# Optimization experiments

Hardware: AMD Instinct MI355X
Metric: run time of the kernel (lower is better)

Reference implementation:

```python
import jax, jax.numpy as jnp
import numpy as np

B, N_IN, D_IN, N_OUT, D_OUT, ROUTINGS = 512, 1152, 8, 10, 16, 3


def squash(s, axis=-1):
    # scale = |s|^2 / (1 + |s|^2) / (|s| + 1e-8)
    norm = jnp.linalg.norm(s, axis=axis, keepdims=True)
    return (norm ** 2 / (1.0 + norm ** 2) / (norm + 1e-8)) * s


def setup_inputs() -> dict:
    key = jax.random.key(0)
    k1, k2 = jax.random.split(key)
    x = jax.random.normal(k1, (B, N_IN, D_IN), dtype=jnp.float32)
    weight = 0.01 * jax.random.normal(k2, (N_OUT, N_IN, D_OUT, D_IN), dtype=jnp.float32)
    return {"x": x, "weight": weight}


def reference(x, weight):
    # x: [B, N_IN, D_IN]; weight: [N_OUT, N_IN, D_OUT, D_IN]
    # x_hat[b,o,n,:] = weight[o,n] @ x[b,n]  -> [B, N_OUT, N_IN, D_OUT]
    x_hat = jnp.einsum('onij,bnj->boni', weight, x)
    x_hat_det = jax.lax.stop_gradient(x_hat)

    # routing logits b: [B, N_OUT, N_IN]
    b = jnp.zeros(x_hat.shape[:3], dtype=x_hat.dtype)
    outputs = None
    for i in range(ROUTINGS):
        c = jax.nn.softmax(b, axis=1)  # softmax over output capsules
        if i == ROUTINGS - 1:
            outputs = squash(jnp.sum(c[..., None] * x_hat, axis=2))  # [B, N_OUT, D_OUT]
        else:
            outputs = squash(jnp.sum(c[..., None] * x_hat_det, axis=2))
            # agreement: b += <outputs, x_hat_det> over D_OUT
            b = b + jnp.einsum('bod,bond->bon', outputs, x_hat_det)
    return outputs  # [B, N_OUT, D_OUT]
```

## Files before the change

### kernel.cpp

```cpp
#include <hip/hip_runtime.h>
#include <hip/hip_bf16.h>

#define B_    512
#define NI    1152
#define NO    10
#define BT    16
#define NBT   32
#define NC    24
#define NCH   48
#define RNDS  6
#define RN    8

#define WBUF_US 12288
#define BUF_US  13312

typedef __attribute__((ext_vector_type(8))) short bf16x8;
typedef __attribute__((ext_vector_type(4))) float f32x4;
typedef __attribute__((ext_vector_type(8))) unsigned short u16x8;

#define SPART_F32  ((size_t)NC * NBT * NO * 256)
#define OUTSUM_F32 ((size_t)NBT * NO * 256)
#define XB_US      ((size_t)NBT * NC * RNDS * 1024)
#define WB_US      ((size_t)NC * RNDS * WBUF_US)

__device__ inline unsigned short f2bf(float f) {
    __hip_bfloat16 h = __float2bfloat16(f);
    return *reinterpret_cast<unsigned short*>(&h);
}

__device__ inline void gld_lds16(const void* g, void* lds) {
    __builtin_amdgcn_global_load_lds(
        (const __attribute__((address_space(1))) void*)g,
        (__attribute__((address_space(3))) void*)lds, 16, 0, 0);
}

__global__ __launch_bounds__(256) void cvt_xw(
    const float* __restrict__ x, const float* __restrict__ w,
    unsigned short* __restrict__ xb, unsigned short* __restrict__ wb)
{
    const int blk = blockIdx.x;
    if (blk < 2304) {
        const int t   = blk * 256 + threadIdx.x;
        const int m   = t & 127;
        const int img = t >> 7;
        const int nl  = m >> 4, bl = m & 15;
        const int r   = img % RNDS;
        const int bc  = img / RNDS;
        const int nc  = bc % NC, bt = bc / NC;
        const int b   = bt * BT + bl;
        const int n   = nc * NCH + r * RN + nl;
        const float* src = x + ((size_t)b * NI + n) * 8;
        float4 v0 = *reinterpret_cast<const float4*>(src);
        float4 v1 = *reinterpret_cast<const float4*>(src + 4);
        u16x8 u = { f2bf(v0.x), f2bf(v0.y), f2bf(v0.z), f2bf(v0.w),
                    f2bf(v1.x), f2bf(v1.y), f2bf(v1.z), f2bf(v1.w) };
        *reinterpret_cast<u16x8*>(xb + (size_t)t * 8) = u;
    } else {
        const int t    = (blk - 2304) * 256 + threadIdx.x;
        const int lane = t & 63;
        const int gs   = (t >> 6) % 24;
        const int img  = t / 1536;
        const int hi   = lane >> 4, d = lane & 15;
        const int nl   = gs / 3, oq = gs % 3;
        const int r    = img % RNDS, nc = img / RNDS;
        const int o    = oq * 4 + hi;
        const int n    = nc * NCH + r * RN + nl;
        u16x8 u = {0,0,0,0,0,0,0,0};
        if (o < NO) {
            const float* src = w + ((size_t)o * NI + n) * 128 + d * 8;
            float4 v0 = *reinterpret_cast<const float4*>(src);
            float4 v1 = *reinterpret_cast<const float4*>(src + 4);
            u = (u16x8){ f2bf(v0.x), f2bf(v0.y), f2bf(v0.z), f2bf(v0.w),
                         f2bf(v1.x), f2bf(v1.y), f2bf(v1.z), f2bf(v1.w) };
        }
        *reinterpret_cast<u16x8*>(wb + (size_t)t * 8) = u;
    }
}

template<bool UNIFORM>
__global__ __launch_bounds__(256, 3) void caps_iter(
    const unsigned short* __restrict__ xb,
    const unsigned short* __restrict__ wb,
    const float* __restrict__ outsum,
    float* __restrict__ s_part)
{
    __shared__ unsigned short lds[2 * BUF_US];

    const int tid = threadIdx.x;
    const int w   = tid >> 6;
    const int l   = tid & 63;
    const int b16 = l & 15;
    const int hi  = l >> 4;
    const int blk = blockIdx.x;
    const int xcd = blk & 7, idx = blk >> 3;
    const int nc  = xcd * 3 + (idx >> 5);
    const int bt  = idx & 31;

    const unsigned short* wsrc = wb + (size_t)nc * (RNDS * WBUF_US);
    const unsigned short* xsrc = xb + ((size_t)bt * NC + nc) * (RNDS * 1024);

    auto stage = [&](int r, int kbuf) {
        const unsigned short* wr = wsrc + (size_t)r * WBUF_US;
        char* dst = (char*)lds + kbuf * (BUF_US * 2);
        #pragma unroll
        for (int k = 0; k < 6; ++k)
            gld_lds16(wr + (k * 256 + tid) * 8, dst + (k * 256 + tid) * 16);
        if (tid < 128)
            gld_lds16(xsrc + (size_t)r * 1024 + tid * 8,
                      dst + WBUF_US * 2 + tid * 16);
    };

    f32x4 outf[NO];
    if constexpr (!UNIFORM) {
        #pragma unroll
        for (int o = 0; o < NO; ++o)
            outf[o] = *reinterpret_cast<const f32x4*>(
                outsum + (((size_t)bt * NO + o) * 64 + l) * 4);
    }

    f32x4 sacc[NO];
    #pragma unroll
    for (int o = 0; o < NO; ++o) sacc[o] = (f32x4){0.f, 0.f, 0.f, 0.f};

    stage(0, 0);
    asm volatile("s_waitcnt vmcnt(0)" ::: "memory");
    __syncthreads();

    #pragma unroll 1
    for (int r = 0; r < RNDS; ++r) {
        if (r + 1 < RNDS) stage(r + 1, (r + 1) & 1);

        const int ub = (r & 1) * BUF_US;

        #pragma unroll 1
        for (int i = 0; i < 2; ++i) {
            const int nl = w * 2 + i;
            bf16x8 bv = *reinterpret_cast<const bf16x8*>(
                &lds[ub + WBUF_US + nl * 128 + b16 * 8]);
            bf16x8 bvt[4];
            #pragma unroll
            for (int t = 0; t < 4; ++t)
                bvt[t] = (hi == t) ? bv : (bf16x8){0,0,0,0,0,0,0,0};

            if constexpr (UNIFORM) {
                #pragma unroll
                for (int oq = 0; oq < 3; ++oq) {
                    bf16x8 av = *reinterpret_cast<const bf16x8*>(
                        &lds[ub + (nl * 3 + oq) * 512 + l * 8]);
                    const int tmax = (oq < 2) ? 4 : 2;
                    #pragma unroll
                    for (int t = 0; t < tmax; ++t)
                        sacc[oq * 4 + t] = __builtin_amdgcn_mfma_f32_16x16x32_bf16(
                            av, bvt[t], sacc[oq * 4 + t], 0, 0, 0);
                }
            } else {
                float lg[NO];
                #pragma unroll
                for (int oq = 0; oq < 3; ++oq) {
                    bf16x8 av = *reinterpret_cast<const bf16x8*>(
                        &lds[ub + (nl * 3 + oq) * 512 + l * 8]);
                    const int tmax = (oq < 2) ? 4 : 2;
                    #pragma unroll
                    for (int t = 0; t < tmax; ++t) {
                        f32x4 xh = __builtin_amdgcn_mfma_f32_16x16x32_bf16(
                            av, bvt[t], (f32x4){0.f, 0.f, 0.f, 0.f}, 0, 0, 0);
                        const int o = oq * 4 + t;
                        float pp = outf[o][0] * xh[0];
                        pp = fmaf(outf[o][1], xh[1], pp);
                        pp = fmaf(outf[o][2], xh[2], pp);
                        pp = fmaf(outf[o][3], xh[3], pp);
                        pp += __shfl_xor(pp, 16, 64);
                        pp += __shfl_xor(pp, 32, 64);
                        lg[o] = pp;
                    }
                }
                float sum = 0.f;
                #pragma unroll
                for (int o = 0; o < NO; ++o) { lg[o] = __expf(lg[o]); sum += lg[o]; }
                const float rs = __builtin_amdgcn_rcpf(sum);
                #pragma unroll
                for (int oq = 0; oq < 3; ++oq) {
                    bf16x8 av = *reinterpret_cast<const bf16x8*>(
                        &lds[ub + (nl * 3 + oq) * 512 + l * 8]);
                    const int tmax = (oq < 2) ? 4 : 2;
                    #pragma unroll
                    for (int t = 0; t < tmax; ++t) {
                        f32x4 xh = __builtin_amdgcn_mfma_f32_16x16x32_bf16(
                            av, bvt[t], (f32x4){0.f, 0.f, 0.f, 0.f}, 0, 0, 0);
                        const int o = oq * 4 + t;
                        const float cc = lg[o] * rs;
                        sacc[o][0] = fmaf(cc, xh[0], sacc[o][0]);
                        sacc[o][1] = fmaf(cc, xh[1], sacc[o][1]);
                        sacc[o][2] = fmaf(cc, xh[2], sacc[o][2]);
                        sacc[o][3] = fmaf(cc, xh[3], sacc[o][3]);
                    }
                }
            }
        }

        asm volatile("s_waitcnt vmcnt(0)" ::: "memory");
        __syncthreads();
    }

    const float sc = UNIFORM ? 0.1f : 1.0f;
    f32x4* red = reinterpret_cast<f32x4*>(lds);
    #pragma unroll
    for (int o = 0; o < NO; ++o)
        red[w * 640 + o * 64 + l] =
            (f32x4){sacc[o][0] * sc, sacc[o][1] * sc,
                    sacc[o][2] * sc, sacc[o][3] * sc};
    __syncthreads();
    float* base = s_part + ((size_t)nc * NBT + bt) * 2560;
    for (int g = tid; g < 640; g += 256) {
        f32x4 a0 = red[g], a1 = red[640 + g], a2 = red[1280 + g], a3 = red[1920 + g];
        f32x4 s;
        #pragma unroll
        for (int q = 0; q < 4; ++q) s[q] = (a0[q] + a1[q]) + (a2[q] + a3[q]);
        *reinterpret_cast<f32x4*>(base + (size_t)g * 4) = s;
    }
}

template<int MODE>
__global__ __launch_bounds__(256) void caps_squash(
    const float* __restrict__ s_part,
    float* __restrict__ outsum,
    float* __restrict__ dout)
{
    __shared__ float sq[256];
    const int bo = blockIdx.x;
    const int t  = threadIdx.x;

    float s = 0.f;
    #pragma unroll
    for (int nc = 0; nc < NC; ++nc)
        s += s_part[((size_t)nc * NBT * NO + bo) * 256 + t];

    float n2 = s * s;
    n2 += __shfl_xor(n2, 1, 64);
    n2 += __shfl_xor(n2, 2, 64);
    sq[t] = n2;
    __syncthreads();
    const int base = t & 63;
    n2 = (sq[base] + sq[64 + base]) + (sq[128 + base] + sq[192 + base]);

    const float norm  = sqrtf(n2);
    const float scale = n2 / ((1.f + n2) * (norm + 1e-8f));
    const float v = scale * s;

    if constexpr (MODE == 0) {
        outsum[(size_t)bo * 256 + t] = v;
    } else if constexpr (MODE == 1) {
        outsum[(size_t)bo * 256 + t] += v;
    } else {
        const int bt = bo / NO, o = bo - bt * NO;
        const int b16 = (t >> 2) & 15, hi = t >> 6, q = t & 3;
        dout[((size_t)(bt * BT + b16) * NO + o) * 16 + hi * 4 + q] = v;
    }
}

extern "C" void kernel_launch(void* const* d_in, const int* in_sizes, int n_in,
                              void* d_out, int out_size, void* d_ws, size_t ws_size,
                              hipStream_t stream) {
    const float* x = (const float*)d_in[0];
    const float* w = (const float*)d_in[1];
    float* out = (float*)d_out;

    float* s_part          = (float*)d_ws;
    float* outsum          = s_part + SPART_F32;
    unsigned short* xb     = (unsigned short*)(outsum + OUTSUM_F32);
    unsigned short* wb     = xb + XB_US;

    cvt_xw<<<dim3(3168), dim3(256), 0, stream>>>(x, w, xb, wb);

    dim3 gI(NBT * NC), bI(256);
    dim3 gS(NBT * NO), bS(256);

    caps_iter<true ><<<gI, bI, 0, stream>>>(xb, wb, nullptr, s_part);
    caps_squash<0><<<gS, bS, 0, stream>>>(s_part, outsum, nullptr);
    caps_iter<false><<<gI, bI, 0, stream>>>(xb, wb, outsum, s_part);
    caps_squash<1><<<gS, bS, 0, stream>>>(s_part, outsum, nullptr);
    caps_iter<false><<<gI, bI, 0, stream>>>(xb, wb, outsum, s_part);
    caps_squash<2><<<gS, bS, 0, stream>>>(s_part, nullptr, out);
}
```

Measured before the change: 77.91 us.

## Halve per-round staging, raise occupancy, store partial sums in fp16

Splits each chunk into 12 rounds of 4 input capsules so each wave handles one capsule per round, which halves the LDS staging buffers and allows 4 blocks per CU. The per-block partial sums and the LDS reduction buffer now use fp16, halving the s_part traffic written by caps_iter and read by caps_squash. The cost is more rounds and barriers per block, and fp16 rounding of partial sums, which adds precision risk.

Measured after the change: 102.5 us. +31.5%, slower.

```diff
diff --git a/kernel.cpp b/kernel.cpp
--- a/kernel.cpp
+++ b/kernel.cpp
@@ -1,5 +1,6 @@
 #include <hip/hip_runtime.h>
 #include <hip/hip_bf16.h>
+#include <hip/hip_fp16.h>
 
 #define B_    512
 #define NI    1152
@@ -8,19 +9,20 @@
 #define NBT   32
 #define NC    24
 #define NCH   48
-#define RNDS  6
-#define RN    8
-
-#define WBUF_US 12288
-#define BUF_US  13312
+#define RNDS  12
+#define RN    4
+
+#define WBUF_US 6144
+#define XBUF_US 512
+#define BUF_US  6656
 
 typedef __attribute__((ext_vector_type(8))) short bf16x8;
 typedef __attribute__((ext_vector_type(4))) float f32x4;
 typedef __attribute__((ext_vector_type(8))) unsigned short u16x8;
 
-#define SPART_F32  ((size_t)NC * NBT * NO * 256)
+#define SPART_H    ((size_t)NC * NBT * NO * 256)
 #define OUTSUM_F32 ((size_t)NBT * NO * 256)
-#define XB_US      ((size_t)NBT * NC * RNDS * 1024)
+#define XB_US      ((size_t)NBT * NC * RNDS * XBUF_US)
 #define WB_US      ((size_t)NC * RNDS * WBUF_US)
 
 __device__ inline unsigned short f2bf(float f) {
@@ -41,8 +43,8 @@
     const int blk = blockIdx.x;
     if (blk < 2304) {
         const int t   = blk * 256 + threadIdx.x;
-        const int m   = t & 127;
-        const int img = t >> 7;
+        const int m   = t & 63;
+        const int img = t >> 6;
         const int nl  = m >> 4, bl = m & 15;
         const int r   = img % RNDS;
         const int bc  = img / RNDS;
@@ -58,8 +60,8 @@
     } else {
         const int t    = (blk - 2304) * 256 + threadIdx.x;
         const int lane = t & 63;
-        const int gs   = (t >> 6) % 24;
-        const int img  = t / 1536;
+        const int gs   = (t >> 6) % 12;
+        const int img  = t / 768;
         const int hi   = lane >> 4, d = lane & 15;
         const int nl   = gs / 3, oq = gs % 3;
         const int r    = img % RNDS, nc = img / RNDS;
@@ -77,14 +79,19 @@
     }
 }
 
+union LdsU {
+    unsigned short stage[2 * BUF_US];
+    uint2 red[4][NO * 64];
+};
+
 template<bool UNIFORM>
-__global__ __launch_bounds__(256, 3) void caps_iter(
+__global__ __launch_bounds__(256, 4) void caps_iter(
     const unsigned short* __restrict__ xb,
     const unsigned short* __restrict__ wb,
     const float* __restrict__ outsum,
-    float* __restrict__ s_part)
+    unsigned short* __restrict__ s_part)
 {
-    __shared__ unsigned short lds[2 * BUF_US];
+    __shared__ LdsU lds;
 
     const int tid = threadIdx.x;
     const int w   = tid >> 6;
@@ -97,16 +104,16 @@
     const int bt  = idx & 31;
 
     const unsigned short* wsrc = wb + (size_t)nc * (RNDS * WBUF_US);
-    const unsigned short* xsrc = xb + ((size_t)bt * NC + nc) * (RNDS * 1024);
+    const unsigned short* xsrc = xb + ((size_t)bt * NC + nc) * (RNDS * XBUF_US);
 
     auto stage = [&](int r, int kbuf) {
         const unsigned short* wr = wsrc + (size_t)r * WBUF_US;
-        char* dst = (char*)lds + kbuf * (BUF_US * 2);
+        char* dst = (char*)lds.stage + kbuf * (BUF_US * 2);
         #pragma unroll
-        for (int k = 0; k < 6; ++k)
+        for (int k = 0; k < 3; ++k)
             gld_lds16(wr + (k * 256 + tid) * 8, dst + (k * 256 + tid) * 16);
-        if (tid < 128)
-            gld_lds16(xsrc + (size_t)r * 1024 + tid * 8,
+        if (tid < 64)
+            gld_lds16(xsrc + (size_t)r * XBUF_US + tid * 8,
                       dst + WBUF_US * 2 + tid * 16);
     };
 
@@ -132,68 +139,64 @@
 
         const int ub = (r & 1) * BUF_US;
 
-        #pragma unroll 1
-        for (int i = 0; i < 2; ++i) {
-            const int nl = w * 2 + i;
-            bf16x8 bv = *reinterpret_cast<const bf16x8*>(
-                &lds[ub + WBUF_US + nl * 128 + b16 * 8]);
-            bf16x8 bvt[4];
+        bf16x8 bv = *reinterpret_cast<const bf16x8*>(
+            &lds.stage[ub + WBUF_US + w * 128 + b16 * 8]);
+        bf16x8 bvt[4];
+        #pragma unroll
+        for (int t = 0; t < 4; ++t)
+            bvt[t] = (hi == t) ? bv : (bf16x8){0,0,0,0,0,0,0,0};
+
+        if constexpr (UNIFORM) {
             #pragma unroll
-            for (int t = 0; t < 4; ++t)
-                bvt[t] = (hi == t) ? bv : (bf16x8){0,0,0,0,0,0,0,0};
-
-            if constexpr (UNIFORM) {
+            for (int oq = 0; oq < 3; ++oq) {
+                bf16x8 av = *reinterpret_cast<const bf16x8*>(
+                    &lds.stage[ub + (w * 3 + oq) * 512 + l * 8]);
+                const int tmax = (oq < 2) ? 4 : 2;
                 #pragma unroll
-                for (int oq = 0; oq < 3; ++oq) {
-                    bf16x8 av = *reinterpret_cast<const bf16x8*>(
-                        &lds[ub + (nl * 3 + oq) * 512 + l * 8]);
-                    const int tmax = (oq < 2) ? 4 : 2;
-                    #pragma unroll
-                    for (int t = 0; t < tmax; ++t)
-                        sacc[oq * 4 + t] = __builtin_amdgcn_mfma_f32_16x16x32_bf16(
-                            av, bvt[t], sacc[oq * 4 + t], 0, 0, 0);
+                for (int t = 0; t < tmax; ++t)
+                    sacc[oq * 4 + t] = __builtin_amdgcn_mfma_f32_16x16x32_bf16(
+                        av, bvt[t], sacc[oq * 4 + t], 0, 0, 0);
+            }
+        } else {
+            float lg[NO];
+            #pragma unroll
+            for (int oq = 0; oq < 3; ++oq) {
+                bf16x8 av = *reinterpret_cast<const bf16x8*>(
+                    &lds.stage[ub + (w * 3 + oq) * 512 + l * 8]);
+                const int tmax = (oq < 2) ? 4 : 2;
+                #pragma unroll
+                for (int t = 0; t < tmax; ++t) {
+                    f32x4 xh = __builtin_amdgcn_mfma_f32_16x16x32_bf16(
+                        av, bvt[t], (f32x4){0.f, 0.f, 0.f, 0.f}, 0, 0, 0);
+                    const int o = oq * 4 + t;
+                    float pp = outf[o][0] * xh[0];
+                    pp = fmaf(outf[o][1], xh[1], pp);
+                    pp = fmaf(outf[o][2], xh[2], pp);
+                    pp = fmaf(outf[o][3], xh[3], pp);
+                    pp += __shfl_xor(pp, 16, 64);
+                    pp += __shfl_xor(pp, 32, 64);
+                    lg[o] = pp;
                 }
-            } else {
-                float lg[NO];
+            }
+            float sum = 0.f;
+            #pragma unroll
+            for (int o = 0; o < NO; ++o) { lg[o] = __expf(lg[o]); sum += lg[o]; }
+            const float rs = __builtin_amdgcn_rcpf(sum);
+            #pragma unroll
+            for (int oq = 0; oq < 3; ++oq) {
+                bf16x8 av = *reinterpret_cast<const bf16x8*>(
+                    &lds.stage[ub + (w * 3 + oq) * 512 + l * 8]);
+                const int tmax = (oq < 2) ? 4 : 2;
                 #pragma unroll
-                for (int oq = 0; oq < 3; ++oq) {
-                    bf16x8 av = *reinterpret_cast<const bf16x8*>(
-                        &lds[ub + (nl * 3 + oq) * 512 + l * 8]);
-                    const int tmax = (oq < 2) ? 4 : 2;
-                    #pragma unroll
-                    for (int t = 0; t < tmax; ++t) {
-                        f32x4 xh = __builtin_amdgcn_mfma_f32_16x16x32_bf16(
-                            av, bvt[t], (f32x4){0.f, 0.f, 0.f, 0.f}, 0, 0, 0);
-                        const int o = oq * 4 + t;
-                        float pp = outf[o][0] * xh[0];
-                        pp = fmaf(outf[o][1], xh[1], pp);
-                        pp = fmaf(outf[o][2], xh[2], pp);
-                        pp = fmaf(outf[o][3], xh[3], pp);
-                        pp += __shfl_xor(pp, 16, 64);
-                        pp += __shfl_xor(pp, 32, 64);
-                        lg[o] = pp;
-                    }
-                }
-                float sum = 0.f;
-                #pragma unroll
-                for (int o = 0; o < NO; ++o) { lg[o] = __expf(lg[o]); sum += lg[o]; }
-                const float rs = __builtin_amdgcn_rcpf(sum);
-                #pragma unroll
-                for (int oq = 0; oq < 3; ++oq) {
-                    bf16x8 av = *reinterpret_cast<const bf16x8*>(
-                        &lds[ub + (nl * 3 + oq) * 512 + l * 8]);
-                    const int tmax = (oq < 2) ? 4 : 2;
-                    #pragma unroll
-                    for (int t = 0; t < tmax; ++t) {
-                        f32x4 xh = __builtin_amdgcn_mfma_f32_16x16x32_bf16(
-                            av, bvt[t], (f32x4){0.f, 0.f, 0.f, 0.f}, 0, 0, 0);
-                        const int o = oq * 4 + t;
-                        const float cc = lg[o] * rs;
-                        sacc[o][0] = fmaf(cc, xh[0], sacc[o][0]);
-                        sacc[o][1] = fmaf(cc, xh[1], sacc[o][1]);
-                        sacc[o][2] = fmaf(cc, xh[2], sacc[o][2]);
-                        sacc[o][3] = fmaf(cc, xh[3], sacc[o][3]);
-                    }
+                for (int t = 0; t < tmax; ++t) {
+                    f32x4 xh = __builtin_amdgcn_mfma_f32_16x16x32_bf16(
+                        av, bvt[t], (f32x4){0.f, 0.f, 0.f, 0.f}, 0, 0, 0);
+                    const int o = oq * 4 + t;
+                    const float cc = lg[o] * rs;
+                    sacc[o][0] = fmaf(cc, xh[0], sacc[o][0]);
+                    sacc[o][1] = fmaf(cc, xh[1], sacc[o][1]);
+                    sacc[o][2] = fmaf(cc, xh[2], sacc[o][2]);
+                    sacc[o][3] = fmaf(cc, xh[3], sacc[o][3]);
                 }
             }
         }
@@ -203,26 +206,38 @@
     }
 
     const float sc = UNIFORM ? 0.1f : 1.0f;
-    f32x4* red = reinterpret_cast<f32x4*>(lds);
     #pragma unroll
-    for (int o = 0; o < NO; ++o)
-        red[w * 640 + o * 64 + l] =
-            (f32x4){sacc[o][0] * sc, sacc[o][1] * sc,
-                    sacc[o][2] * sc, sacc[o][3] * sc};
+    for (int o = 0; o < NO; ++o) {
+        __half2 h01 = __floats2half2_rn(sacc[o][0] * sc, sacc[o][1] * sc);
+        __half2 h23 = __floats2half2_rn(sacc[o][2] * sc, sacc[o][3] * sc);
+        lds.red[w][o * 64 + l] =
+            make_uint2(*reinterpret_cast<unsigned int*>(&h01),
+                       *reinterpret_cast<unsigned int*>(&h23));
+    }
     __syncthreads();
-    float* base = s_part + ((size_t)nc * NBT + bt) * 2560;
-    for (int g = tid; g < 640; g += 256) {
-        f32x4 a0 = red[g], a1 = red[640 + g], a2 = red[1280 + g], a3 = red[1920 + g];
-        f32x4 s;
-        #pragma unroll
-        for (int q = 0; q < 4; ++q) s[q] = (a0[q] + a1[q]) + (a2[q] + a3[q]);
-        *reinterpret_cast<f32x4*>(base + (size_t)g * 4) = s;
+    unsigned short* base = s_part + ((size_t)nc * NBT + bt) * 2560;
+    for (int g = tid; g < NO * 64; g += 256) {
+        uint2 a0 = lds.red[0][g], a1 = lds.red[1][g],
+              a2 = lds.red[2][g], a3 = lds.red[3][g];
+        auto h2f2 = [](unsigned int u) {
+            __half2 h = *reinterpret_cast<__half2*>(&u);
+            return __half22float2(h);
+        };
+        float2 lo = h2f2(a0.x), l1 = h2f2(a1.x), l2 = h2f2(a2.x), l3 = h2f2(a3.x);
+        float2 ho = h2f2(a0.y), h1 = h2f2(a1.y), h2 = h2f2(a2.y), h3 = h2f2(a3.y);
+        float2 sl = { (lo.x + l1.x) + (l2.x + l3.x), (lo.y + l1.y) + (l2.y + l3.y) };
+        float2 sh = { (ho.x + h1.x) + (h2.x + h3.x), (ho.y + h1.y) + (h2.y + h3.y) };
+        __half2 p01 = __floats2half2_rn(sl.x, sl.y);
+        __half2 p23 = __floats2half2_rn(sh.x, sh.y);
+        *reinterpret_cast<uint2*>(base + (size_t)g * 4) =
+            make_uint2(*reinterpret_cast<unsigned int*>(&p01),
+                       *reinterpret_cast<unsigned int*>(&p23));
     }
 }
 
 template<int MODE>
 __global__ __launch_bounds__(256) void caps_squash(
-    const float* __restrict__ s_part,
+    const unsigned short* __restrict__ s_part,
     float* __restrict__ outsum,
     float* __restrict__ dout)
 {
@@ -231,9 +246,12 @@
     const int t  = threadIdx.x;
 
     float s = 0.f;
-    #pragma unroll
-    for (int nc = 0; nc < NC; ++nc)
-        s += s_part[((size_t)nc * NBT * NO + bo) * 256 + t];
+    #pragma unroll 4
+    for (int nc = 0; nc < NC; ++nc) {
+        __half h = *reinterpret_cast<const __half*>(
+            s_part + ((size_t)nc * NBT * NO + bo) * 256 + t);
+        s += __half2float(h);
+    }
 
     float n2 = s * s;
     n2 += __shfl_xor(n2, 1, 64);
@@ -265,8 +283,8 @@
     const float* w = (const float*)d_in[1];
     float* out = (float*)d_out;
 
-    float* s_part          = (float*)d_ws;
-    float* outsum          = s_part + SPART_F32;
+    unsigned short* s_part = (unsigned short*)d_ws;
+    float*          outsum = (float*)(s_part + SPART_H);
     unsigned short* xb     = (unsigned short*)(outsum + OUTSUM_F32);
     unsigned short* wb     = xb + XB_US;
 
```
